# Optimization experiments

Measured on AMD Instinct MI355X. Metric: run time of the kernel, lower is better.

## Reference

```python
import jax, jax.numpy as jnp
import numpy as np

NC, ND = 100000, 100000
E, L = 500000, 100000
HID, OUT = 128, 64
NH, HD = 4, 32
NL = 2


def setup_inputs() -> dict:
    key = jax.random.key(0)
    ks = jax.random.split(key, 16)
    f = jnp.float32
    s_lin = 1.0 / np.sqrt(HID)
    s_rel = 1.0 / np.sqrt(HD)
    return {
        "emb_C": jax.random.normal(ks[0], (NC, HID), f) * 0.1,
        "emb_D": jax.random.normal(ks[1], (ND, HID), f) * 0.1,
        "kW": jax.random.normal(ks[2], (NL, 2, HID, HID), f) * s_lin,
        "kb": jnp.zeros((NL, 2, HID), f),
        "qW": jax.random.normal(ks[3], (NL, 2, HID, HID), f) * s_lin,
        "qb": jnp.zeros((NL, 2, HID), f),
        "vW": jax.random.normal(ks[4], (NL, 2, HID, HID), f) * s_lin,
        "vb": jnp.zeros((NL, 2, HID), f),
        "aW": jax.random.normal(ks[5], (NL, 2, HID, HID), f) * s_lin,
        "ab": jnp.zeros((NL, 2, HID), f),
        "skip": jnp.ones((NL, 2), f),
        "arel": jax.random.normal(ks[6], (NL, 2, NH, HD, HD), f) * s_rel,
        "mrel": jax.random.normal(ks[7], (NL, 2, NH, HD, HD), f) * s_rel,
        "prel": jnp.ones((NL, 2, NH), f),
        "outW": jax.random.normal(ks[8], (2, HID, OUT), f) * s_lin,
        "outb": jnp.zeros((2, OUT), f),
        # edge_index for (Compound -> Disease) and reverse (Disease -> Compound)
        "ei_cd": jnp.stack([jax.random.randint(ks[9], (E,), 0, NC),
                            jax.random.randint(ks[10], (E,), 0, ND)]).astype(jnp.int32),
        "ei_dc": jnp.stack([jax.random.randint(ks[11], (E,), 0, ND),
                            jax.random.randint(ks[12], (E,), 0, NC)]).astype(jnp.int32),
        # edge_label_index: (Compound, Disease) pairs to score
        "eli": jnp.stack([jax.random.randint(ks[13], (L,), 0, NC),
                          jax.random.randint(ks[14], (L,), 0, ND)]).astype(jnp.int32),
    }


def _seg_softmax(a, seg, n):
    # numerically stable softmax over edges grouped by destination node
    amax = jax.ops.segment_max(a, seg, num_segments=n)
    amax = jnp.where(jnp.isfinite(amax), amax, 0.0)
    ex = jnp.exp(a - amax[seg])
    den = jax.ops.segment_sum(ex, seg, num_segments=n)
    return ex / (den[seg] + 1e-16)


def _hgt_layer(xs, p, ei_cd, ei_dc):
    kW, kb, qW, qb, vW, vb, aW, ab, skip, arel, mrel, prel = p
    # per-node-type K/Q/V projections, reshaped to [N, heads, head_dim]
    k = [(xs[t] @ kW[t] + kb[t]).reshape(-1, NH, HD) for t in range(2)]
    q = [(xs[t] @ qW[t] + qb[t]).reshape(-1, NH, HD) for t in range(2)]
    v = [(xs[t] @ vW[t] + vb[t]).reshape(-1, NH, HD) for t in range(2)]
    outs = [jnp.zeros_like(k[0]), jnp.zeros_like(k[1])]
    rels = [(0, 1, ei_cd), (1, 0, ei_dc)]  # (src_type, dst_type, edge_index)
    for r, (s, d, ei) in enumerate(rels):
        # relation-specific transforms applied per source node (as in PyG HGTConv)
        krel = jnp.einsum('nhd,hde->nhe', k[s], arel[r])
        vrel = jnp.einsum('nhd,hde->nhe', v[s], mrel[r])
        src, dst = ei[0], ei[1]
        ndst = xs[d].shape[0]
        a = (q[d][dst] * krel[src]).sum(-1) * prel[r] / np.sqrt(HD)  # [E, NH]
        alpha = _seg_softmax(a, dst, ndst)
        msg = vrel[src] * alpha[..., None]                           # [E, NH, HD]
        outs[d] = outs[d] + jax.ops.segment_sum(msg, dst, num_segments=ndst)
    new = []
    for t in range(2):
        o = outs[t].reshape(-1, HID)
        o = jax.nn.gelu(o) @ aW[t] + ab[t]
        g = jax.nn.sigmoid(skip[t])
        new.append(g * o + (1.0 - g) * xs[t])  # skip connection (in==out dims)
    return new


def reference(emb_C, emb_D, kW, kb, qW, qb, vW, vb, aW, ab, skip, arel, mrel, prel,
              outW, outb, ei_cd, ei_dc, eli):
    xs = [emb_C, emb_D]
    for l in range(NL):
        p = (kW[l], kb[l], qW[l], qb[l], vW[l], vb[l], aW[l], ab[l],
             skip[l], arel[l], mrel[l], prel[l])
        xs = _hgt_layer(xs, p, ei_cd, ei_dc)
        xs = [jax.nn.relu(x) for x in xs]  # dropout(0.2) in eval mode -> identity
    zC = xs[0] @ outW[0] + outb[0]
    zD = xs[1] @ outW[1] + outb[1]
    logits = jnp.clip((zC[eli[0]] * zD[eli[1]]).sum(-1), -10.0, 10.0)
    return logits
```

## Files before the change

### kernel.cpp

```cpp
#include <hip/hip_runtime.h>
#include <math.h>

#define NC_   100000
#define ND_   100000
#define NN_   100000
#define E_CNT 500000
#define L_CNT 100000
#define NH_   4
#define HD_   32
#define WCAT_SZ (129 * 384)

__device__ __forceinline__ float gelu_f(float x) {
    const float c0 = 0.7978845608028654f;
    float x3 = x * x * x;
    return 0.5f * x * (1.0f + tanhf(c0 * (x + 0.044715f * x3)));
}

__global__ __launch_bounds__(256) void fill0_int(int* __restrict__ p, int n) {
    int i = blockIdx.x * 256 + threadIdx.x;
    if (i < n) p[i] = 0;
}

__global__ __launch_bounds__(256) void count_dst(const int* __restrict__ dstA,
                                                 const int* __restrict__ dstB,
                                                 int* __restrict__ cnt) {
    int r = blockIdx.y;
    const int* dst = r ? dstB : dstA;
    int e = blockIdx.x * 256 + threadIdx.x;
    if (e < E_CNT) atomicAdd(&cnt[r * NN_ + dst[e]], 1);
}

__global__ __launch_bounds__(256) void scan_a(const int* __restrict__ cnt,
                                              int* __restrict__ excl,
                                              int* __restrict__ partials) {
    __shared__ int sd[256];
    int r = blockIdx.y;
    cnt += r * NN_; excl += r * (NN_ + 1); partials += r * 128;
    int b = blockIdx.x, t = threadIdx.x;
    int base = b * 1024 + t * 4;
    int v0 = (base + 0 < NN_) ? cnt[base + 0] : 0;
    int v1 = (base + 1 < NN_) ? cnt[base + 1] : 0;
    int v2 = (base + 2 < NN_) ? cnt[base + 2] : 0;
    int v3 = (base + 3 < NN_) ? cnt[base + 3] : 0;
    int tsum = v0 + v1 + v2 + v3;
    sd[t] = tsum; __syncthreads();
    for (int off = 1; off < 256; off <<= 1) {
        int x = (t >= off) ? sd[t - off] : 0;
        __syncthreads();
        sd[t] += x;
        __syncthreads();
    }
    int excl_t = sd[t] - tsum;
    if (t == 255) partials[b] = sd[t];
    int q = excl_t;
    if (base + 0 < NN_) excl[base + 0] = q; q += v0;
    if (base + 1 < NN_) excl[base + 1] = q; q += v1;
    if (base + 2 < NN_) excl[base + 2] = q; q += v2;
    if (base + 3 < NN_) excl[base + 3] = q;
}

__global__ __launch_bounds__(128) void scan_b(int* __restrict__ partials) {
    __shared__ int sd[128];
    partials += blockIdx.x * 128;
    int t = threadIdx.x;
    int orig = (t < 98) ? partials[t] : 0;
    sd[t] = orig; __syncthreads();
    for (int off = 1; off < 128; off <<= 1) {
        int x = (t >= off) ? sd[t - off] : 0;
        __syncthreads();
        sd[t] += x;
        __syncthreads();
    }
    if (t < 98) partials[t] = sd[t] - orig;
}

__global__ __launch_bounds__(256) void scan_c(int* __restrict__ row_ptr,
                                              const int* __restrict__ partials,
                                              int* __restrict__ cursor) {
    int r = blockIdx.y;
    row_ptr += r * (NN_ + 1); partials += r * 128; cursor += r * NN_;
    int b = blockIdx.x, t = threadIdx.x;
    int base = b * 1024 + t * 4;
    int add = partials[b];
    #pragma unroll
    for (int j = 0; j < 4; j++) {
        int i = base + j;
        if (i < NN_) { int v = row_ptr[i] + add; row_ptr[i] = v; cursor[i] = v; }
    }
    if (b == 0 && t == 0) row_ptr[NN_] = E_CNT;
}

__global__ __launch_bounds__(256) void scatter_edges(const int* __restrict__ srcA,
                                                     const int* __restrict__ dstA,
                                                     const int* __restrict__ srcB,
                                                     const int* __restrict__ dstB,
                                                     int* __restrict__ cursor,
                                                     int* __restrict__ srcs) {
    int r = blockIdx.y;
    const int* src = r ? srcB : srcA;
    const int* dst = r ? dstB : dstA;
    cursor += r * NN_; srcs += r * E_CNT;
    int e = blockIdx.x * 256 + threadIdx.x;
    if (e >= E_CNT) return;
    int pos = atomicAdd(&cursor[dst[e]], 1);
    srcs[pos] = src[e];
}

__global__ void fuse_weights(const float* __restrict__ qW, const float* __restrict__ qb,
                             const float* __restrict__ kW, const float* __restrict__ kb,
                             const float* __restrict__ vW, const float* __restrict__ vb,
                             const float* __restrict__ arel, const float* __restrict__ mrel,
                             float* __restrict__ WcatAll)
{
    int i  = blockIdx.x;
    int t  = blockIdx.y;
    int lyr = blockIdx.z;
    int oc = threadIdx.x;
    int lt = lyr * 2 + t;
    float* Wcat = WcatAll + (size_t)lt * WCAT_SZ;
    float val;
    if (oc < 128) {
        val = (i < 128) ? qW[(size_t)(lt * 128 + i) * 128 + oc] : qb[lt * 128 + oc];
    } else {
        int which = (oc >= 256);
        int cc = oc - (which ? 256 : 128);
        int h = cc >> 5, e = cc & 31;
        const float* W = which ? vW : kW;
        const float* b = which ? vb : kb;
        const float* R = (which ? mrel : arel) + (size_t)(lt * NH_ + h) * HD_ * HD_ + e;
        float s = 0.f;
        if (i < 128) {
            const float* wrow = W + (size_t)(lt * 128 + i) * 128 + h * 32;
            #pragma unroll
            for (int d2 = 0; d2 < 32; d2++) s += wrow[d2] * R[d2 * 32];
        } else {
            const float* brow = b + lt * 128 + h * 32;
            #pragma unroll
            for (int d2 = 0; d2 < 32; d2++) s += brow[d2] * R[d2 * 32];
        }
        val = s;
    }
    Wcat[(size_t)((i < 128) ? i : 128) * 384 + oc] = val;
}

template<int TN, int POST>
__global__ __launch_bounds__(256)
void gemm2(const float* __restrict__ A, int lda,
           const float* __restrict__ B, int ldb,
           const float* __restrict__ bias,
           float* __restrict__ C, int ldc,
           int M,
           const float* __restrict__ resid,
           const float* __restrict__ skipv,
           int ySplit,
           const float* __restrict__ A2, const float* __restrict__ B2,
           const float* __restrict__ bias2, float* __restrict__ C2, int ldc2)
{
    constexpr int TC = TN / 16;
    __shared__ float As[2][16][132];
    __shared__ float Bs[2][16][TN + 4];
    int by = blockIdx.y;
    if (ySplit >= 0 && by >= ySplit) {
        A = A2; B = B2; bias = bias2; C = C2; ldc = ldc2; by -= ySplit;
    }
    int tid = threadIdx.x;
    int tx = tid & 15, ty = tid >> 4;
    int bm = blockIdx.x * 128;
    int bn = by * TN;
    float acc[8][TC];
    #pragma unroll
    for (int i = 0; i < 8; i++)
        #pragma unroll
        for (int j = 0; j < TC; j++) acc[i][j] = 0.f;

    int m_a  = tid >> 1;
    int koff = (tid & 1) * 8;
    int arow = bm + m_a;
    bool avalid = arow < M;
    const float* aptr = A + (size_t)arow * lda + koff;
    int k_b = tid >> 4;
    int txs = tid & 15;
    const float* bptr = B + (size_t)k_b * ldb + bn + txs * 4;

    float4 a0 = make_float4(0.f,0.f,0.f,0.f), a1 = a0, b0, b1;
    if (avalid) { a0 = *(const float4*)(aptr); a1 = *(const float4*)(aptr + 4); }
    b0 = *(const float4*)(bptr);
    if (TC == 8) b1 = *(const float4*)(bptr + 64);
    As[0][koff + 0][m_a] = a0.x; As[0][koff + 1][m_a] = a0.y;
    As[0][koff + 2][m_a] = a0.z; As[0][koff + 3][m_a] = a0.w;
    As[0][koff + 4][m_a] = a1.x; As[0][koff + 5][m_a] = a1.y;
    As[0][koff + 6][m_a] = a1.z; As[0][koff + 7][m_a] = a1.w;
    *(float4*)&Bs[0][k_b][txs * 4] = b0;
    if (TC == 8) *(float4*)&Bs[0][k_b][64 + txs * 4] = b1;
    __syncthreads();

    int ibuf = 0;
    for (int k0 = 0; k0 < 128; k0 += 16) {
        bool more = (k0 + 16) < 128;
        if (more) {
            if (avalid) {
                a0 = *(const float4*)(aptr + k0 + 16);
                a1 = *(const float4*)(aptr + k0 + 20);
            }
            b0 = *(const float4*)(bptr + (size_t)(k0 + 16) * ldb);
            if (TC == 8) b1 = *(const float4*)(bptr + (size_t)(k0 + 16) * ldb + 64);
        }
        #pragma unroll
        for (int kk = 0; kk < 16; kk++) {
            float a[8], b[TC];
            *(float4*)&a[0] = *(const float4*)&As[ibuf][kk][ty * 8];
            *(float4*)&a[4] = *(const float4*)&As[ibuf][kk][ty * 8 + 4];
            *(float4*)&b[0] = *(const float4*)&Bs[ibuf][kk][tx * 4];
            if (TC == 8) *(float4*)&b[4] = *(const float4*)&Bs[ibuf][kk][64 + tx * 4];
            #pragma unroll
            for (int i = 0; i < 8; i++)
                #pragma unroll
                for (int j = 0; j < TC; j++)
                    acc[i][j] += a[i] * b[j];
        }
        if (more) {
            int nb = ibuf ^ 1;
            As[nb][koff + 0][m_a] = a0.x; As[nb][koff + 1][m_a] = a0.y;
            As[nb][koff + 2][m_a] = a0.z; As[nb][koff + 3][m_a] = a0.w;
            As[nb][koff + 4][m_a] = a1.x; As[nb][koff + 5][m_a] = a1.y;
            As[nb][koff + 6][m_a] = a1.z; As[nb][koff + 7][m_a] = a1.w;
            *(float4*)&Bs[nb][k_b][txs * 4] = b0;
            if (TC == 8) *(float4*)&Bs[nb][k_b][64 + txs * 4] = b1;
            __syncthreads();
            ibuf = nb;
        }
    }

    float g = 0.f, omg = 0.f;
    if (POST) { float sv = skipv[0]; g = 1.0f / (1.0f + expf(-sv)); omg = 1.0f - g; }
    float bb[TC];
    #pragma unroll
    for (int j = 0; j < 4; j++) bb[j] = bias[bn + tx * 4 + j];
    if (TC == 8)
        #pragma unroll
        for (int j = 0; j < 4; j++) bb[4 + j] = bias[bn + 64 + tx * 4 + j];
    #pragma unroll
    for (int i = 0; i < 8; i++) {
        int m = bm + ty * 8 + i;
        if (m >= M) continue;
        #pragma unroll
        for (int half = 0; half < TC / 4; half++) {
            int coff = bn + half * 64 + tx * 4;
            float* crow = C + (size_t)m * ldc + coff;
            float4 v;
            v.x = acc[i][half * 4 + 0] + bb[half * 4 + 0];
            v.y = acc[i][half * 4 + 1] + bb[half * 4 + 1];
            v.z = acc[i][half * 4 + 2] + bb[half * 4 + 2];
            v.w = acc[i][half * 4 + 3] + bb[half * 4 + 3];
            if (POST) {
                float4 r = *(const float4*)(resid + (size_t)m * ldc + coff);
                v.x = fmaxf(g * v.x + omg * r.x, 0.f);
                v.y = fmaxf(g * v.y + omg * r.y, 0.f);
                v.z = fmaxf(g * v.z + omg * r.z, 0.f);
                v.w = fmaxf(g * v.w + omg * r.w, 0.f);
            }
            *(float4*)crow = v;
        }
    }
}

__global__ __launch_bounds__(256)
void attn_gather(const int* __restrict__ row_ptr, const int* __restrict__ srcs,
                 float* __restrict__ qo, const float* __restrict__ kv,
                 const float* __restrict__ prel, int ndst)
{
    int wave = (blockIdx.x * 256 + threadIdx.x) >> 6;
    int lane = threadIdx.x & 63;
    if (wave >= ndst) return;
    int d = wave;
    int gl = lane & 15;
    int group = lane >> 4;
    int h = gl >> 2;
    float pr = prel[h] * 0.17677669529663687f;
    int beg = row_ptr[d], end = row_ptr[d + 1];
    const float* qrow = qo + (size_t)d * 128 + gl * 8;
    float4 q0 = *(const float4*)(qrow);
    float4 q1 = *(const float4*)(qrow + 4);
    float m = -1.0e30f, l = 0.f;
    float4 acc0 = make_float4(0.f,0.f,0.f,0.f), acc1 = acc0;
    int nt = (end - beg + 3) >> 2;
    for (int t = 0; t < nt; t++) {
        int i = beg + (t << 2) + group;
        if (i < end) {
            int s = srcs[i];
            const float* row = kv + (size_t)s * 256 + gl * 8;
            float4 k0 = *(const float4*)(row);
            float4 k1 = *(const float4*)(row + 4);
            float4 v0 = *(const float4*)(row + 128);
            float4 v1 = *(const float4*)(row + 132);
            float part = q0.x*k0.x + q0.y*k0.y + q0.z*k0.z + q0.w*k0.w
                       + q1.x*k1.x + q1.y*k1.y + q1.z*k1.z + q1.w*k1.w;
            part += __shfl_xor(part, 1);
            part += __shfl_xor(part, 2);
            float a = part * pr;
            float mn = fmaxf(m, a);
            float scale = expf(m - mn);
            float p = expf(a - mn);
            l = l * scale + p;
            acc0.x = acc0.x * scale + p * v0.x;
            acc0.y = acc0.y * scale + p * v0.y;
            acc0.z = acc0.z * scale + p * v0.z;
            acc0.w = acc0.w * scale + p * v0.w;
            acc1.x = acc1.x * scale + p * v1.x;
            acc1.y = acc1.y * scale + p * v1.y;
            acc1.z = acc1.z * scale + p * v1.z;
            acc1.w = acc1.w * scale + p * v1.w;
            m = mn;
        }
    }
    #pragma unroll
    for (int mask = 16; mask <= 32; mask <<= 1) {
        float m_o = __shfl_xor(m, mask);
        float l_o = __shfl_xor(l, mask);
        float4 a0o, a1o;
        a0o.x = __shfl_xor(acc0.x, mask); a0o.y = __shfl_xor(acc0.y, mask);
        a0o.z = __shfl_xor(acc0.z, mask); a0o.w = __shfl_xor(acc0.w, mask);
        a1o.x = __shfl_xor(acc1.x, mask); a1o.y = __shfl_xor(acc1.y, mask);
        a1o.z = __shfl_xor(acc1.z, mask); a1o.w = __shfl_xor(acc1.w, mask);
        float mn = fmaxf(m, m_o);
        float s0 = expf(m - mn), s1 = expf(m_o - mn);
        l = l * s0 + l_o * s1;
        acc0.x = acc0.x * s0 + a0o.x * s1; acc0.y = acc0.y * s0 + a0o.y * s1;
        acc0.z = acc0.z * s0 + a0o.z * s1; acc0.w = acc0.w * s0 + a0o.w * s1;
        acc1.x = acc1.x * s0 + a1o.x * s1; acc1.y = acc1.y * s0 + a1o.y * s1;
        acc1.z = acc1.z * s0 + a1o.z * s1; acc1.w = acc1.w * s0 + a1o.w * s1;
        m = mn;
    }
    float inv = (beg == end) ? 0.f : 1.f / (l + 1e-16f);
    if (group == 0) {
        float* orow = qo + (size_t)d * 128 + gl * 8;
        float4 o0, o1;
        o0.x = gelu_f(acc0.x * inv); o0.y = gelu_f(acc0.y * inv);
        o0.z = gelu_f(acc0.z * inv); o0.w = gelu_f(acc0.w * inv);
        o1.x = gelu_f(acc1.x * inv); o1.y = gelu_f(acc1.y * inv);
        o1.z = gelu_f(acc1.z * inv); o1.w = gelu_f(acc1.w * inv);
        *(float4*)(orow)     = o0;
        *(float4*)(orow + 4) = o1;
    }
}

__global__ __launch_bounds__(256)
void score_pairs(const int* __restrict__ ic, const int* __restrict__ id,
                 const float* __restrict__ zC, const float* __restrict__ zD,
                 float* __restrict__ out)
{
    int gid = blockIdx.x * 256 + threadIdx.x;
    int p = gid >> 4, lane = gid & 15;
    if (p >= L_CNT) return;
    int c = ic[p], d = id[p];
    float4 a = *(const float4*)(zC + (size_t)c * 64 + lane * 4);
    float4 b = *(const float4*)(zD + (size_t)d * 64 + lane * 4);
    float s = a.x * b.x + a.y * b.y + a.z * b.z + a.w * b.w;
    s += __shfl_down(s, 8, 16);
    s += __shfl_down(s, 4, 16);
    s += __shfl_down(s, 2, 16);
    s += __shfl_down(s, 1, 16);
    if (lane == 0) out[p] = fminf(10.0f, fmaxf(-10.0f, s));
}

extern "C" void kernel_launch(void* const* d_in, const int* in_sizes, int n_in,
                              void* d_out, int out_size, void* d_ws, size_t ws_size,
                              hipStream_t stream)
{
    float* xC = (float*)d_in[0];
    float* xD = (float*)d_in[1];
    const float* kW   = (const float*)d_in[2];
    const float* kb   = (const float*)d_in[3];
    const float* qW   = (const float*)d_in[4];
    const float* qb   = (const float*)d_in[5];
    const float* vW   = (const float*)d_in[6];
    const float* vb   = (const float*)d_in[7];
    const float* aW   = (const float*)d_in[8];
    const float* ab   = (const float*)d_in[9];
    const float* skip = (const float*)d_in[10];
    const float* arel = (const float*)d_in[11];
    const float* mrel = (const float*)d_in[12];
    const float* prel = (const float*)d_in[13];
    const float* outW = (const float*)d_in[14];
    const float* outb = (const float*)d_in[15];
    const int* ei_cd  = (const int*)d_in[16];
    const int* ei_dc  = (const int*)d_in[17];
    const int* eli    = (const int*)d_in[18];

    float* ws = (float*)d_ws;
    size_t off = 0;
    float* kv    = ws + off; off += (size_t)NN_ * 256;
    float* qo    = ws + off; off += (size_t)NN_ * 128;
    float* Wcat  = ws + off; off += (size_t)4 * WCAT_SZ;
    int* iws = (int*)(ws + off);
    size_t ioff = 0;
    int* rp      = iws + ioff; ioff += 2 * (NN_ + 1);
    int* srcsA   = iws + ioff; ioff += 2 * E_CNT;
    int* cnt     = iws + ioff; ioff += 2 * NN_;
    int* cursor  = iws + ioff; ioff += 2 * NN_;
    int* partial = iws + ioff; ioff += 256;
    float* zC = kv;
    float* zD = kv + (size_t)NN_ * 128;

    const int gridM = (NN_ + 127) / 128;
    const int gE    = (E_CNT + 255) / 256;
    const int gN2   = (2 * NN_ + 255) / 256;
    const int gScan = 98;
    const int gGath = (NN_ + 3) / 4;

    fill0_int<<<gN2, 256, 0, stream>>>(cnt, 2 * NN_);
    count_dst<<<dim3(gE, 2), 256, 0, stream>>>(ei_cd + E_CNT, ei_dc + E_CNT, cnt);
    scan_a<<<dim3(gScan, 2), 256, 0, stream>>>(cnt, rp, partial);
    scan_b<<<2, 128, 0, stream>>>(partial);
    scan_c<<<dim3(gScan, 2), 256, 0, stream>>>(rp, partial, cursor);
    scatter_edges<<<dim3(gE, 2), 256, 0, stream>>>(ei_cd, ei_cd + E_CNT,
                                                   ei_dc, ei_dc + E_CNT, cursor, srcsA);
    int* rp_cd   = rp;
    int* rp_dc   = rp + (NN_ + 1);
    int* srcs_cd = srcsA;
    int* srcs_dc = srcsA + E_CNT;

    fuse_weights<<<dim3(129, 2, 2), 384, 0, stream>>>(qW, qb, kW, kb, vW, vb,
                                                      arel, mrel, Wcat);

    for (int l = 0; l < 2; l++) {
        const float* aWl = aW + (size_t)l * 2 * 128 * 128;
        const float* abl = ab + (size_t)l * 2 * 128;
        float* WcC = Wcat + (size_t)(l * 2 + 0) * WCAT_SZ;
        float* WcD = Wcat + (size_t)(l * 2 + 1) * WCAT_SZ;

        gemm2<128, 0><<<dim3(gridM, 3), 256, 0, stream>>>(
            xC, 128, WcC + 128, 384, WcC + 128 * 384 + 128, kv, 256, NC_, nullptr, nullptr,
            2, xD, WcD, WcD + 128 * 384, qo, 128);
        attn_gather<<<gGath, 256, 0, stream>>>(rp_cd, srcs_cd, qo, kv,
                                               prel + (l * 2 + 0) * 4, ND_);

        gemm2<128, 0><<<dim3(gridM, 2), 256, 0, stream>>>(
            xD, 128, WcD + 128, 384, WcD + 128 * 384 + 128, kv, 256, ND_, nullptr, nullptr,
            -1, nullptr, nullptr, nullptr, nullptr, 0);

        gemm2<128, 1><<<dim3(gridM, 1), 256, 0, stream>>>(
            qo, 128, aWl + 128 * 128, 128, abl + 128, xD, 128, ND_, xD, skip + l * 2 + 1,
            -1, nullptr, nullptr, nullptr, nullptr, 0);

        gemm2<128, 0><<<dim3(gridM, 1), 256, 0, stream>>>(
            xC, 128, WcC, 384, WcC + 128 * 384, qo, 128, NC_, nullptr, nullptr,
            -1, nullptr, nullptr, nullptr, nullptr, 0);
        attn_gather<<<gGath, 256, 0, stream>>>(rp_dc, srcs_dc, qo, kv,
                                               prel + (l * 2 + 1) * 4, NC_);

        gemm2<128, 1><<<dim3(gridM, 1), 256, 0, stream>>>(
            qo, 128, aWl, 128, abl, xC, 128, NC_, xC, skip + l * 2 + 0,
            -1, nullptr, nullptr, nullptr, nullptr, 0);
    }

    gemm2<64, 0><<<dim3(gridM, 2), 256, 0, stream>>>(
        xC, 128, outW, 64, outb, zC, 64, NC_, nullptr, nullptr,
        1, xD, outW + 128 * 64, outb + 64, zD, 64);

    score_pairs<<<(L_CNT * 16 + 255) / 256, 256, 0, stream>>>(
        eli, eli + L_CNT, zC, zD, (float*)d_out);
}
```

Baseline: 1.445 ms.

## Replace FP32 SIMT GEMMs with split-bf16 MFMA GEMMs

Replaces the scalar FP32 tiled GEMM with a matrix-core kernel. Each FP32 operand is split into three bf16 parts and six bf16 MFMA products are accumulated to approximate FP32 accuracy. Weights are pre-split once by a new kernel, and activations are split on the fly in shared memory with a 64-row tile. The aim is to move the projection GEMM work onto matrix cores, at the cost of extra split arithmetic, sixfold MFMA work, unvectorised scalar epilogue stores and a little residual precision loss.

Result: faster. 1.268 ms (-12.3%).

```diff
diff --git a/kernel.cpp b/kernel.cpp
--- a/kernel.cpp
+++ b/kernel.cpp
@@ -10,10 +10,22 @@
 #define HD_   32
 #define WCAT_SZ (129 * 384)
 
+typedef __attribute__((ext_vector_type(8))) short short8;
+typedef __attribute__((ext_vector_type(4))) float floatx4;
+
 __device__ __forceinline__ float gelu_f(float x) {
     const float c0 = 0.7978845608028654f;
     float x3 = x * x * x;
     return 0.5f * x * (1.0f + tanhf(c0 * (x + 0.044715f * x3)));
+}
+
+__device__ __forceinline__ unsigned short bf_rne(float x) {
+    unsigned int u = __float_as_uint(x);
+    u += 0x7fffu + ((u >> 16) & 1u);
+    return (unsigned short)(u >> 16);
+}
+__device__ __forceinline__ float bf_to_f(unsigned short b) {
+    return __uint_as_float(((unsigned int)b) << 16);
 }
 
 __global__ __launch_bounds__(256) void fill0_int(int* __restrict__ p, int n) {
@@ -143,123 +155,134 @@
     Wcat[(size_t)((i < 128) ? i : 128) * 384 + oc] = val;
 }
 
+__global__ __launch_bounds__(128)
+void split_w(const float* __restrict__ W, int ldw, int matStride,
+             unsigned short* __restrict__ out, int N, int outMatStride)
+{
+    int n = blockIdx.x;
+    int mat = blockIdx.y;
+    int k = threadIdx.x;
+    float x = W[(size_t)mat * matStride + (size_t)k * ldw + n];
+    unsigned short b0 = bf_rne(x);
+    float x1 = x - bf_to_f(b0);
+    unsigned short b1 = bf_rne(x1);
+    float x2 = x1 - bf_to_f(b1);
+    unsigned short b2 = bf_rne(x2);
+    int ps = N * 128;
+    unsigned short* o = out + (size_t)mat * outMatStride + (size_t)n * 128 + k;
+    o[0] = b0; o[ps] = b1; o[2 * ps] = b2;
+}
+
 template<int TN, int POST>
 __global__ __launch_bounds__(256)
-void gemm2(const float* __restrict__ A, int lda,
-           const float* __restrict__ B, int ldb,
-           const float* __restrict__ bias,
-           float* __restrict__ C, int ldc,
-           int M,
-           const float* __restrict__ resid,
-           const float* __restrict__ skipv,
-           int ySplit,
-           const float* __restrict__ A2, const float* __restrict__ B2,
-           const float* __restrict__ bias2, float* __restrict__ C2, int ldc2)
+void gemm_mfma(const float* __restrict__ A, int lda,
+               const unsigned short* __restrict__ Bs3, int pstride,
+               const float* __restrict__ bias,
+               float* __restrict__ C, int ldc, int M,
+               const float* __restrict__ resid, const float* __restrict__ skipv,
+               int ySplit,
+               const float* __restrict__ A2, const unsigned short* __restrict__ Bs32,
+               int pstride2, const float* __restrict__ bias2,
+               float* __restrict__ C2, int ldc2)
 {
-    constexpr int TC = TN / 16;
-    __shared__ float As[2][16][132];
-    __shared__ float Bs[2][16][TN + 4];
+    constexpr int CT = TN / 16;
+    __shared__ unsigned short Asl[3 * 64 * 40];
+    __shared__ unsigned short Bsl[3 * TN * 40];
     int by = blockIdx.y;
     if (ySplit >= 0 && by >= ySplit) {
-        A = A2; B = B2; bias = bias2; C = C2; ldc = ldc2; by -= ySplit;
-    }
-    int tid = threadIdx.x;
-    int tx = tid & 15, ty = tid >> 4;
-    int bm = blockIdx.x * 128;
+        A = A2; Bs3 = Bs32; pstride = pstride2; bias = bias2; C = C2; ldc = ldc2;
+        by -= ySplit;
+    }
+    int tid  = threadIdx.x;
+    int wave = tid >> 6, lane = tid & 63;
+    int quad = lane >> 4, l16 = lane & 15;
+    int bm = blockIdx.x * 64;
     int bn = by * TN;
-    float acc[8][TC];
+
+    floatx4 acc[CT];
     #pragma unroll
-    for (int i = 0; i < 8; i++)
+    for (int ct = 0; ct < CT; ct++) acc[ct] = (floatx4){0.f, 0.f, 0.f, 0.f};
+
+    int sm = tid >> 2;
+    int kq = (tid & 3) * 8;
+    int arow = bm + sm;
+    bool aval = arow < M;
+    const float* ap = A + (size_t)arow * lda + kq;
+    int sn = tid >> 1;
+    int kh = (tid & 1) * 16;
+    const unsigned short* bp = Bs3 + (size_t)(bn + sn) * 128 + kh;
+
+    for (int ks = 0; ks < 128; ks += 32) {
+        __syncthreads();
+        float xv[8];
+        if (aval) {
+            *(float4*)&xv[0] = *(const float4*)(ap + ks);
+            *(float4*)&xv[4] = *(const float4*)(ap + ks + 4);
+        } else {
+            #pragma unroll
+            for (int i = 0; i < 8; i++) xv[i] = 0.f;
+        }
         #pragma unroll
-        for (int j = 0; j < TC; j++) acc[i][j] = 0.f;
-
-    int m_a  = tid >> 1;
-    int koff = (tid & 1) * 8;
-    int arow = bm + m_a;
-    bool avalid = arow < M;
-    const float* aptr = A + (size_t)arow * lda + koff;
-    int k_b = tid >> 4;
-    int txs = tid & 15;
-    const float* bptr = B + (size_t)k_b * ldb + bn + txs * 4;
-
-    float4 a0 = make_float4(0.f,0.f,0.f,0.f), a1 = a0, b0, b1;
-    if (avalid) { a0 = *(const float4*)(aptr); a1 = *(const float4*)(aptr + 4); }
-    b0 = *(const float4*)(bptr);
-    if (TC == 8) b1 = *(const float4*)(bptr + 64);
-    As[0][koff + 0][m_a] = a0.x; As[0][koff + 1][m_a] = a0.y;
-    As[0][koff + 2][m_a] = a0.z; As[0][koff + 3][m_a] = a0.w;
-    As[0][koff + 4][m_a] = a1.x; As[0][koff + 5][m_a] = a1.y;
-    As[0][koff + 6][m_a] = a1.z; As[0][koff + 7][m_a] = a1.w;
-    *(float4*)&Bs[0][k_b][txs * 4] = b0;
-    if (TC == 8) *(float4*)&Bs[0][k_b][64 + txs * 4] = b1;
-    __syncthreads();
-
-    int ibuf = 0;
-    for (int k0 = 0; k0 < 128; k0 += 16) {
-        bool more = (k0 + 16) < 128;
-        if (more) {
-            if (avalid) {
-                a0 = *(const float4*)(aptr + k0 + 16);
-                a1 = *(const float4*)(aptr + k0 + 20);
+        for (int i = 0; i < 8; i += 2) {
+            float xa = xv[i], xb = xv[i + 1];
+            unsigned short a0 = bf_rne(xa); float ra = xa - bf_to_f(a0);
+            unsigned short a1 = bf_rne(ra); float ra2 = ra - bf_to_f(a1);
+            unsigned short a2 = bf_rne(ra2);
+            unsigned short c0 = bf_rne(xb); float rb = xb - bf_to_f(c0);
+            unsigned short c1 = bf_rne(rb); float rb2 = rb - bf_to_f(c1);
+            unsigned short c2 = bf_rne(rb2);
+            int idx = sm * 40 + kq + i;
+            *(unsigned int*)&Asl[idx]            = (unsigned)a0 | ((unsigned)c0 << 16);
+            *(unsigned int*)&Asl[2560 + idx]     = (unsigned)a1 | ((unsigned)c1 << 16);
+            *(unsigned int*)&Asl[5120 + idx]     = (unsigned)a2 | ((unsigned)c2 << 16);
+        }
+        if (sn < TN) {
+            #pragma unroll
+            for (int p = 0; p < 3; p++) {
+                uint4 v0 = *(const uint4*)(bp + (size_t)p * pstride + ks);
+                uint4 v1 = *(const uint4*)(bp + (size_t)p * pstride + ks + 8);
+                int bidx = p * (TN * 40) + sn * 40 + kh;
+                *(uint4*)&Bsl[bidx]     = v0;
+                *(uint4*)&Bsl[bidx + 8] = v1;
             }
-            b0 = *(const float4*)(bptr + (size_t)(k0 + 16) * ldb);
-            if (TC == 8) b1 = *(const float4*)(bptr + (size_t)(k0 + 16) * ldb + 64);
-        }
+        }
+        __syncthreads();
+        int am = wave * 16 + l16;
+        short8 af0 = *(const short8*)&Asl[am * 40 + quad * 8];
+        short8 af1 = *(const short8*)&Asl[2560 + am * 40 + quad * 8];
+        short8 af2 = *(const short8*)&Asl[5120 + am * 40 + quad * 8];
         #pragma unroll
-        for (int kk = 0; kk < 16; kk++) {
-            float a[8], b[TC];
-            *(float4*)&a[0] = *(const float4*)&As[ibuf][kk][ty * 8];
-            *(float4*)&a[4] = *(const float4*)&As[ibuf][kk][ty * 8 + 4];
-            *(float4*)&b[0] = *(const float4*)&Bs[ibuf][kk][tx * 4];
-            if (TC == 8) *(float4*)&b[4] = *(const float4*)&Bs[ibuf][kk][64 + tx * 4];
-            #pragma unroll
-            for (int i = 0; i < 8; i++)
-                #pragma unroll
-                for (int j = 0; j < TC; j++)
-                    acc[i][j] += a[i] * b[j];
-        }
-        if (more) {
-            int nb = ibuf ^ 1;
-            As[nb][koff + 0][m_a] = a0.x; As[nb][koff + 1][m_a] = a0.y;
-            As[nb][koff + 2][m_a] = a0.z; As[nb][koff + 3][m_a] = a0.w;
-            As[nb][koff + 4][m_a] = a1.x; As[nb][koff + 5][m_a] = a1.y;
-            As[nb][koff + 6][m_a] = a1.z; As[nb][koff + 7][m_a] = a1.w;
-            *(float4*)&Bs[nb][k_b][txs * 4] = b0;
-            if (TC == 8) *(float4*)&Bs[nb][k_b][64 + txs * 4] = b1;
-            __syncthreads();
-            ibuf = nb;
+        for (int ct = 0; ct < CT; ct++) {
+            int bnn = (ct * 16 + l16) * 40 + quad * 8;
+            short8 bf0 = *(const short8*)&Bsl[bnn];
+            short8 bf1 = *(const short8*)&Bsl[TN * 40 + bnn];
+            short8 bf2 = *(const short8*)&Bsl[2 * TN * 40 + bnn];
+            acc[ct] = __builtin_amdgcn_mfma_f32_16x16x32_bf16(af0, bf2, acc[ct], 0, 0, 0);
+            acc[ct] = __builtin_amdgcn_mfma_f32_16x16x32_bf16(af1, bf1, acc[ct], 0, 0, 0);
+            acc[ct] = __builtin_amdgcn_mfma_f32_16x16x32_bf16(af2, bf0, acc[ct], 0, 0, 0);
+            acc[ct] = __builtin_amdgcn_mfma_f32_16x16x32_bf16(af0, bf1, acc[ct], 0, 0, 0);
+            acc[ct] = __builtin_amdgcn_mfma_f32_16x16x32_bf16(af1, bf0, acc[ct], 0, 0, 0);
+            acc[ct] = __builtin_amdgcn_mfma_f32_16x16x32_bf16(af0, bf0, acc[ct], 0, 0, 0);
         }
     }
 
     float g = 0.f, omg = 0.f;
     if (POST) { float sv = skipv[0]; g = 1.0f / (1.0f + expf(-sv)); omg = 1.0f - g; }
-    float bb[TC];
     #pragma unroll
-    for (int j = 0; j < 4; j++) bb[j] = bias[bn + tx * 4 + j];
-    if (TC == 8)
+    for (int ct = 0; ct < CT; ct++) {
+        int col = bn + ct * 16 + l16;
+        float bv = bias[col];
         #pragma unroll
-        for (int j = 0; j < 4; j++) bb[4 + j] = bias[bn + 64 + tx * 4 + j];
-    #pragma unroll
-    for (int i = 0; i < 8; i++) {
-        int m = bm + ty * 8 + i;
-        if (m >= M) continue;
-        #pragma unroll
-        for (int half = 0; half < TC / 4; half++) {
-            int coff = bn + half * 64 + tx * 4;
-            float* crow = C + (size_t)m * ldc + coff;
-            float4 v;
-            v.x = acc[i][half * 4 + 0] + bb[half * 4 + 0];
-            v.y = acc[i][half * 4 + 1] + bb[half * 4 + 1];
-            v.z = acc[i][half * 4 + 2] + bb[half * 4 + 2];
-            v.w = acc[i][half * 4 + 3] + bb[half * 4 + 3];
-            if (POST) {
-                float4 r = *(const float4*)(resid + (size_t)m * ldc + coff);
-                v.x = fmaxf(g * v.x + omg * r.x, 0.f);
-                v.y = fmaxf(g * v.y + omg * r.y, 0.f);
-                v.z = fmaxf(g * v.z + omg * r.z, 0.f);
-                v.w = fmaxf(g * v.w + omg * r.w, 0.f);
+        for (int i = 0; i < 4; i++) {
+            int row = bm + wave * 16 + quad * 4 + i;
+            if (row < M) {
+                float v = acc[ct][i] + bv;
+                if (POST) {
+                    float r = resid[(size_t)row * ldc + col];
+                    v = fmaxf(g * v + omg * r, 0.f);
+                }
+                C[(size_t)row * ldc + col] = v;
             }
-            *(float4*)crow = v;
         }
     }
 }
@@ -392,6 +415,9 @@
     float* kv    = ws + off; off += (size_t)NN_ * 256;
     float* qo    = ws + off; off += (size_t)NN_ * 128;
     float* Wcat  = ws + off; off += (size_t)4 * WCAT_SZ;
+    unsigned short* WsCat = (unsigned short*)(ws + off); off += (4 * 3 * 384 * 128) / 2;
+    unsigned short* aWs   = (unsigned short*)(ws + off); off += (4 * 3 * 128 * 128) / 2;
+    unsigned short* outWs = (unsigned short*)(ws + off); off += (2 * 3 * 64 * 128) / 2;
     int* iws = (int*)(ws + off);
     size_t ioff = 0;
     int* rp      = iws + ioff; ioff += 2 * (NN_ + 1);
@@ -402,7 +428,7 @@
     float* zC = kv;
     float* zD = kv + (size_t)NN_ * 128;
 
-    const int gridM = (NN_ + 127) / 128;
+    const int gridM = (NN_ + 63) / 64;
     const int gE    = (E_CNT + 255) / 256;
     const int gN2   = (2 * NN_ + 255) / 256;
     const int gScan = 98;
@@ -422,41 +448,52 @@
 
     fuse_weights<<<dim3(129, 2, 2), 384, 0, stream>>>(qW, qb, kW, kb, vW, vb,
                                                       arel, mrel, Wcat);
+    split_w<<<dim3(384, 4), 128, 0, stream>>>(Wcat, 384, WCAT_SZ, WsCat, 384, 3 * 384 * 128);
+    split_w<<<dim3(128, 4), 128, 0, stream>>>(aW, 128, 128 * 128, aWs, 128, 3 * 128 * 128);
+    split_w<<<dim3(64, 2), 128, 0, stream>>>(outW, 64, 128 * 64, outWs, 64, 3 * 64 * 128);
+
+    const int PS_CAT = 384 * 128;
+    const int PS_AW  = 128 * 128;
+    const int PS_OW  = 64 * 128;
 
     for (int l = 0; l < 2; l++) {
-        const float* aWl = aW + (size_t)l * 2 * 128 * 128;
         const float* abl = ab + (size_t)l * 2 * 128;
         float* WcC = Wcat + (size_t)(l * 2 + 0) * WCAT_SZ;
         float* WcD = Wcat + (size_t)(l * 2 + 1) * WCAT_SZ;
-
-        gemm2<128, 0><<<dim3(gridM, 3), 256, 0, stream>>>(
-            xC, 128, WcC + 128, 384, WcC + 128 * 384 + 128, kv, 256, NC_, nullptr, nullptr,
-            2, xD, WcD, WcD + 128 * 384, qo, 128);
+        const unsigned short* WsC = WsCat + (size_t)(l * 2 + 0) * 3 * PS_CAT;
+        const unsigned short* WsD = WsCat + (size_t)(l * 2 + 1) * 3 * PS_CAT;
+        const unsigned short* aWsD = aWs + (size_t)(l * 2 + 1) * 3 * PS_AW;
+        const unsigned short* aWsC = aWs + (size_t)(l * 2 + 0) * 3 * PS_AW;
+
+        gemm_mfma<128, 0><<<dim3(gridM, 3), 256, 0, stream>>>(
+            xC, 128, WsC + 128 * 128, PS_CAT, WcC + 128 * 384 + 128, kv, 256, NC_,
+            nullptr, nullptr,
+            2, xD, WsD, PS_CAT, WcD + 128 * 384, qo, 128);
         attn_gather<<<gGath, 256, 0, stream>>>(rp_cd, srcs_cd, qo, kv,
                                                prel + (l * 2 + 0) * 4, ND_);
 
-        gemm2<128, 0><<<dim3(gridM, 2), 256, 0, stream>>>(
-            xD, 128, WcD + 128, 384, WcD + 128 * 384 + 128, kv, 256, ND_, nullptr, nullptr,
-            -1, nullptr, nullptr, nullptr, nullptr, 0);
-
-        gemm2<128, 1><<<dim3(gridM, 1), 256, 0, stream>>>(
-            qo, 128, aWl + 128 * 128, 128, abl + 128, xD, 128, ND_, xD, skip + l * 2 + 1,
-            -1, nullptr, nullptr, nullptr, nullptr, 0);
-
-        gemm2<128, 0><<<dim3(gridM, 1), 256, 0, stream>>>(
-            xC, 128, WcC, 384, WcC + 128 * 384, qo, 128, NC_, nullptr, nullptr,
-            -1, nullptr, nullptr, nullptr, nullptr, 0);
+        gemm_mfma<128, 0><<<dim3(gridM, 2), 256, 0, stream>>>(
+            xD, 128, WsD + 128 * 128, PS_CAT, WcD + 128 * 384 + 128, kv, 256, ND_,
+            nullptr, nullptr, -1, nullptr, nullptr, 0, nullptr, nullptr, 0);
+
+        gemm_mfma<128, 1><<<dim3(gridM, 1), 256, 0, stream>>>(
+            qo, 128, aWsD, PS_AW, abl + 128, xD, 128, ND_,
+            xD, skip + l * 2 + 1, -1, nullptr, nullptr, 0, nullptr, nullptr, 0);
+
+        gemm_mfma<128, 0><<<dim3(gridM, 1), 256, 0, stream>>>(
+            xC, 128, WsC, PS_CAT, WcC + 128 * 384, qo, 128, NC_,
+            nullptr, nullptr, -1, nullptr, nullptr, 0, nullptr, nullptr, 0);
         attn_gather<<<gGath, 256, 0, stream>>>(rp_dc, srcs_dc, qo, kv,
                                                prel + (l * 2 + 1) * 4, NC_);
 
-        gemm2<128, 1><<<dim3(gridM, 1), 256, 0, stream>>>(
-            qo, 128, aWl, 128, abl, xC, 128, NC_, xC, skip + l * 2 + 0,
-            -1, nullptr, nullptr, nullptr, nullptr, 0);
-    }
-
-    gemm2<64, 0><<<dim3(gridM, 2), 256, 0, stream>>>(
-        xC, 128, outW, 64, outb, zC, 64, NC_, nullptr, nullptr,
-        1, xD, outW + 128 * 64, outb + 64, zD, 64);
+        gemm_mfma<128, 1><<<dim3(gridM, 1), 256, 0, stream>>>(
+            qo, 128, aWsC, PS_AW, abl, xC, 128, NC_,
+            xC, skip + l * 2 + 0, -1, nullptr, nullptr, 0, nullptr, nullptr, 0);
+    }
+
+    gemm_mfma<64, 0><<<dim3(gridM, 2), 256, 0, stream>>>(
+        xC, 128, outWs, PS_OW, outb, zC, 64, NC_, nullptr, nullptr,
+        1, xD, outWs + 3 * PS_OW, PS_OW, outb + 64, zD, 64);
 
     score_pairs<<<(L_CNT * 16 + 255) / 256, 256, 0, stream>>>(
         eli, eli + L_CNT, zC, zD, (float*)d_out);
```
